# Optimization experiments

Measured on AMD Instinct MI355X. Metric: run time of the kernel, lower is better.

## Reference

```python
import jax, jax.numpy as jnp
import numpy as np

B, S, D = 2, 1024, 2048
L = 4
HQ, HKV, HD = 32, 8, 64
I = 5632
V = 32000
EPS = 1e-5
THETA = 10000.0
SCALE = HD ** -0.5
GROUP = HQ // HKV


def setup_inputs() -> dict:
    key = jax.random.key(0)
    ks = jax.random.split(key, 8)
    s = 0.02
    return {
        "input_ids": jax.random.randint(ks[0], (B, S), 0, V, dtype=jnp.int32),
        "positions": jnp.broadcast_to(jnp.arange(S, dtype=jnp.int32), (B, S)),
        "embed": jax.random.normal(ks[1], (V, D), jnp.float32) * s,
        "w_qkv": jax.random.normal(ks[2], (L, D, (HQ + 2 * HKV) * HD), jnp.float32) * s,
        "w_o": jax.random.normal(ks[3], (L, HQ * HD, D), jnp.float32) * s,
        "w_gate_up": jax.random.normal(ks[4], (L, D, 2 * I), jnp.float32) * s,
        "w_down": jax.random.normal(ks[5], (L, I, D), jnp.float32) * s,
        "ln1_w": jnp.ones((L, D), jnp.float32),
        "ln2_w": jnp.ones((L, D), jnp.float32),
        "norm_w": jnp.ones((D,), jnp.float32),
    }


def rmsnorm(x, w):
    var = jnp.mean(x * x, axis=-1, keepdims=True)
    return x * jax.lax.rsqrt(var + EPS) * w


def rope(positions, x):
    # x: [B, S, H, HD]; neox-style rotate-half RoPE
    inv_freq = 1.0 / (THETA ** (jnp.arange(0, HD, 2, dtype=jnp.float32) / HD))
    ang = positions.astype(jnp.float32)[..., None] * inv_freq  # [B, S, HD/2]
    cos = jnp.cos(ang)[:, :, None, :]
    sin = jnp.sin(ang)[:, :, None, :]
    x1, x2 = jnp.split(x, 2, axis=-1)
    return jnp.concatenate([x1 * cos - x2 * sin, x2 * cos + x1 * sin], axis=-1)


def llama_forward(input_ids, positions, embed, w_qkv, w_o, w_gate_up, w_down,
                  ln1_w, ln2_w, norm_w):
    h = embed[input_ids]                      # [B, S, D]
    res = jnp.zeros_like(h)
    causal = jnp.tril(jnp.ones((S, S), dtype=bool))
    neg = jnp.asarray(jnp.finfo(h.dtype).min, h.dtype)

    def layer(carry, params):
        h, res = carry
        wqkv, wo, wgu, wd, l1, l2 = params
        # fused RMSNorm + residual-add (vllm RMSNorm(x, residual) semantics)
        res = h + res
        h = rmsnorm(res, l1)
        # QKV projection + RoPE
        qkv = h @ wqkv
        q, k, v = jnp.split(qkv, [HQ * HD, (HQ + HKV) * HD], axis=-1)
        q = q.reshape(B, S, HQ, HD)
        k = k.reshape(B, S, HKV, HD)
        v = v.reshape(B, S, HKV, HD)
        q = rope(positions, q)
        k = rope(positions, k)
        # GQA: broadcast kv heads across query groups
        k = jnp.repeat(k, GROUP, axis=2)      # [B, S, HQ, HD]
        v = jnp.repeat(v, GROUP, axis=2)
        scores = jnp.einsum('bqhd,bkhd->bhqk', q, k) * SCALE
        scores = jnp.where(causal, scores, neg)
        attn = jax.nn.softmax(scores, axis=-1)
        o = jnp.einsum('bhqk,bkhd->bqhd', attn, v).reshape(B, S, HQ * HD)
        h = o @ wo
        # post-attention fused RMSNorm + residual
        res = h + res
        h = rmsnorm(res, l2)
        # SwiGLU MLP
        gu = h @ wgu
        g, u = jnp.split(gu, 2, axis=-1)
        h = (jax.nn.silu(g) * u) @ wd
        return (h, res), None

    (h, res), _ = jax.lax.scan(layer, (h, res),
                               (w_qkv, w_o, w_gate_up, w_down, ln1_w, ln2_w))
    return rmsnorm(h + res, norm_w)


def reference(input_ids, positions, embed, w_qkv, w_o, w_gate_up, w_down,
              ln1_w, ln2_w, norm_w):
    return llama_forward(input_ids, positions, embed, w_qkv, w_o, w_gate_up,
                         w_down, ln1_w, ln2_w, norm_w)
```

## Files before the change

kernel.cpp:

```cpp
#include <hip/hip_runtime.h>
#include <hip/hip_bf16.h>

#define B_ 2
#define S_ 1024
#define T_ (B_*S_)
#define D_ 2048
#define L_ 4
#define HQ_ 32
#define HKV_ 8
#define HD_ 64
#define I_ 5632
#define EPS_ 1e-5f
#define SCALE_ 0.125f

typedef __attribute__((ext_vector_type(4))) float  float4v;
typedef __attribute__((ext_vector_type(8))) short  short8v;

#define GLOAD16(g, l) \
  __builtin_amdgcn_global_load_lds((const __attribute__((address_space(1))) void*)(g), \
                                   (__attribute__((address_space(3))) void*)(l), 16, 0, 0)

__device__ __forceinline__ short f2bf(float f) {
  union { float f; unsigned u; } c; c.f = f;
  unsigned u = c.u + 0x7fffu + ((c.u >> 16) & 1u);
  return (short)(u >> 16);
}

__device__ __forceinline__ void xcd_swizzle(int gx, int gy, int& bx, int& by) {
  int nwg = gx * gy;
  int orig = by * gx + bx;
  int q = nwg >> 3, r = nwg & 7;
  int xcd = orig & 7, loc = orig >> 3;
  int swz = (xcd < r ? xcd * (q + 1) : r * (q + 1) + (xcd - r) * q) + loc;
  bx = swz / gy;
  by = swz - bx * gy;
}

__global__ __launch_bounds__(256)
void transpose_bf16(const float* __restrict__ in, short* __restrict__ out,
                    int K, int N) {
  __shared__ float t[64][65];
  const int bx = blockIdx.x * 64;
  const int by = blockIdx.y * 64;
  const int tid = threadIdx.x;
  const int lr = tid >> 4;
  const int lc = (tid & 15) * 4;
  #pragma unroll
  for (int j = 0; j < 64; j += 16) {
    float4v v = *(const float4v*)(in + (size_t)(by + lr + j) * N + bx + lc);
    t[lr + j][lc] = v[0]; t[lr + j][lc + 1] = v[1];
    t[lr + j][lc + 2] = v[2]; t[lr + j][lc + 3] = v[3];
  }
  __syncthreads();
  const int nr = tid >> 3;
  const int kc = (tid & 7) * 8;
  #pragma unroll
  for (int j = 0; j < 64; j += 32) {
    short8v y;
    #pragma unroll
    for (int e = 0; e < 8; e++) y[e] = f2bf(t[kc + e][nr + j]);
    *(short8v*)(out + (size_t)(bx + nr + j) * K + by + kc) = y;
  }
}

__global__ __launch_bounds__(256)
void embed_gather(const int* __restrict__ ids, const float* __restrict__ embed,
                  float* __restrict__ h) {
  size_t i = (size_t)blockIdx.x * 256 + threadIdx.x;
  int t  = (int)(i >> 9);
  int d4 = (int)(i & 511);
  ((float4v*)h)[i] = ((const float4v*)(embed + (size_t)ids[t] * D_))[d4];
}

__global__ __launch_bounds__(256)
void rmsnorm_add(const float* __restrict__ x, float* __restrict__ res,
                 const float* __restrict__ w, void* __restrict__ outp,
                 int first, int bf16out) {
  const int row = blockIdx.x;
  const int tid = threadIdx.x;
  const size_t base = (size_t)row * D_;
  float4v v0 = ((const float4v*)(x + base))[tid * 2];
  float4v v1 = ((const float4v*)(x + base))[tid * 2 + 1];
  if (!first) {
    v0 += ((const float4v*)(res + base))[tid * 2];
    v1 += ((const float4v*)(res + base))[tid * 2 + 1];
  }
  ((float4v*)(res + base))[tid * 2]     = v0;
  ((float4v*)(res + base))[tid * 2 + 1] = v1;
  float ss = v0[0]*v0[0] + v0[1]*v0[1] + v0[2]*v0[2] + v0[3]*v0[3]
           + v1[0]*v1[0] + v1[1]*v1[1] + v1[2]*v1[2] + v1[3]*v1[3];
  #pragma unroll
  for (int off = 32; off > 0; off >>= 1) ss += __shfl_xor(ss, off, 64);
  __shared__ float red[4];
  if ((tid & 63) == 0) red[tid >> 6] = ss;
  __syncthreads();
  float tot = red[0] + red[1] + red[2] + red[3];
  float rs = rsqrtf(tot * (1.0f / D_) + EPS_);
  float4v w0 = ((const float4v*)w)[tid * 2];
  float4v w1 = ((const float4v*)w)[tid * 2 + 1];
  float4v o0 = v0 * rs * w0;
  float4v o1 = v1 * rs * w1;
  if (bf16out) {
    short8v y;
    #pragma unroll
    for (int k = 0; k < 4; k++) { y[k] = f2bf(o0[k]); y[k + 4] = f2bf(o1[k]); }
    ((short8v*)((char*)outp + base * 2))[tid] = y;
  } else {
    float* op = (float*)outp + base;
    ((float4v*)op)[tid * 2]     = o0;
    ((float4v*)op)[tid * 2 + 1] = o1;
  }
}

#define BM 128
#define BN 128
#define BKS 32

__global__ __launch_bounds__(512, 2)
void gemm_big(const short* __restrict__ A, const short* __restrict__ Bt,
              float* __restrict__ C, int M, int N, int K) {
  __shared__ short sA[2][128 * 64];
  __shared__ short sB[2][256 * 64];
  int bx = blockIdx.x, by = blockIdx.y;
  xcd_swizzle(gridDim.x, gridDim.y, bx, by);
  const int tid  = threadIdx.x;
  const int lane = tid & 63;
  const int wv   = tid >> 6;
  const int wr   = wv >> 2;
  const int wc   = wv & 3;
  const int row0 = by * 128;
  const int col0 = bx * 256;
  const int fr = lane & 15;
  const int g  = lane >> 4;
  const int NT = K >> 6;

  float4v acc[4][4] = {};

  int rA[2], cA[2], rB[4], cB[4];
  #pragma unroll
  for (int k = 0; k < 2; k++) {
    int s = tid + k * 512;
    rA[k] = s >> 3;
    cA[k] = (((s & 7) ^ (rA[k] & 7)) << 3);
  }
  #pragma unroll
  for (int k = 0; k < 4; k++) {
    int s = tid + k * 512;
    rB[k] = s >> 3;
    cB[k] = (((s & 7) ^ (rB[k] & 7)) << 3);
  }

#define STAGEBIG(t, buf) do { \
    int k0_ = (t) << 6; \
    _Pragma("unroll") \
    for (int k_ = 0; k_ < 2; k_++) \
      GLOAD16(A  + (size_t)(row0 + rA[k_]) * K + k0_ + cA[k_], \
              &sA[buf][(tid + k_ * 512) * 8]); \
    _Pragma("unroll") \
    for (int k_ = 0; k_ < 4; k_++) \
      GLOAD16(Bt + (size_t)(col0 + rB[k_]) * K + k0_ + cB[k_], \
              &sB[buf][(tid + k_ * 512) * 8]); \
  } while (0)

  STAGEBIG(0, 0);

  for (int t = 0; t < NT; t++) {
    const int cur = t & 1;
    if (t + 1 < NT) {
      STAGEBIG(t + 1, cur ^ 1);
      asm volatile("s_waitcnt vmcnt(6)" ::: "memory");
    } else {
      asm volatile("s_waitcnt vmcnt(0)" ::: "memory");
    }
    __builtin_amdgcn_s_barrier();
    __builtin_amdgcn_sched_barrier(0);

    const short* pA = &sA[cur][(wr * 64) * 64];
    const short* pB = &sB[cur][(wc * 64) * 64];
    #pragma unroll
    for (int ks = 0; ks < 2; ks++) {
      const int fswk = ((((ks << 2) | g) ^ (fr & 7)) << 3);
      short8v bfr[4], afr[4];
      #pragma unroll
      for (int ni = 0; ni < 4; ni++)
        bfr[ni] = *(const short8v*)(pB + (ni * 16 + fr) * 64 + fswk);
      #pragma unroll
      for (int m4 = 0; m4 < 4; m4++)
        afr[m4] = *(const short8v*)(pA + (m4 * 16 + fr) * 64 + fswk);
      __builtin_amdgcn_s_setprio(1);
      #pragma unroll
      for (int m4 = 0; m4 < 4; m4++)
        #pragma unroll
        for (int ni = 0; ni < 4; ni++)
          acc[m4][ni] = __builtin_amdgcn_mfma_f32_16x16x32_bf16(
              afr[m4], bfr[ni], acc[m4][ni], 0, 0, 0);
      __builtin_amdgcn_s_setprio(0);
    }
    asm volatile("" ::: "memory");
    __builtin_amdgcn_s_barrier();
  }

  #pragma unroll
  for (int m4 = 0; m4 < 4; m4++)
    #pragma unroll
    for (int ni = 0; ni < 4; ni++) {
      size_t base = (size_t)(row0 + wr * 64 + m4 * 16 + g * 4) * N
                    + col0 + wc * 64 + ni * 16 + fr;
      #pragma unroll
      for (int r = 0; r < 4; r++)
        C[base + (size_t)r * N] = acc[m4][ni][r];
    }
#undef STAGEBIG
}

__global__ __launch_bounds__(256)
void gemm_n64(const short* __restrict__ A, const short* __restrict__ Bt,
              float* __restrict__ C, int M, int N, int K) {
  __shared__ short sA[BM * BKS];
  __shared__ short sB[64 * BKS];
  int bx = blockIdx.x, by = blockIdx.y;
  xcd_swizzle(gridDim.x, gridDim.y, bx, by);
  const int tid  = threadIdx.x;
  const int lane = tid & 63;
  const int wave = tid >> 6;
  const int wm = (wave >> 1) << 6;
  const int wn = (wave & 1) << 5;
  const int row0 = by * BM;
  const int col0 = bx * 64;
  const int fr = lane & 15;
  const int fk = (lane >> 4) << 3;
  float4v acc[4][2] = {};

  const int r_st  = tid >> 2;
  const int kc_st = (tid & 3) << 3;
  const short* pA = A  + (size_t)(row0 + r_st) * K + kc_st;
  const short* pB = Bt + (size_t)(col0 + r_st) * K + kc_st;
  const size_t stride64 = (size_t)64 * K;
  short* lA0 = &sA[tid * 8];
  short* lA1 = &sA[(256 + tid) * 8];
  short* lB0 = &sB[tid * 8];

  for (int k0 = 0; k0 < K; k0 += BKS) {
    GLOAD16(pA, lA0);
    GLOAD16(pA + stride64, lA1);
    GLOAD16(pB, lB0);
    pA += BKS; pB += BKS;
    __syncthreads();
    short8v af[4], bfr[2];
    #pragma unroll
    for (int f = 0; f < 4; f++)
      af[f] = *(const short8v*)(&sA[(wm + f * 16 + fr) * BKS + fk]);
    #pragma unroll
    for (int f = 0; f < 2; f++)
      bfr[f] = *(const short8v*)(&sB[(wn + f * 16 + fr) * BKS + fk]);
    #pragma unroll
    for (int i = 0; i < 4; i++)
      #pragma unroll
      for (int j = 0; j < 2; j++)
        acc[i][j] = __builtin_amdgcn_mfma_f32_16x16x32_bf16(af[i], bfr[j], acc[i][j], 0, 0, 0);
    __syncthreads();
  }
  const int cr = (lane >> 4) << 2;
  const int cc = lane & 15;
  #pragma unroll
  for (int i = 0; i < 4; i++)
    #pragma unroll
    for (int j = 0; j < 2; j++) {
      size_t base = (size_t)(row0 + wm + i * 16 + cr) * N + col0 + wn + j * 16 + cc;
      #pragma unroll
      for (int r = 0; r < 4; r++)
        C[base + (size_t)r * N] = acc[i][j][r];
    }
}

__global__ __launch_bounds__(256)
void gemm_qkv_rope(const short* __restrict__ A, const short* __restrict__ Bt,
                   const float* __restrict__ tab, short* __restrict__ qbf,
                   short* __restrict__ kbf, short* __restrict__ vbf, int K) {
  __shared__ short sA[BM * BKS];
  __shared__ short sB[BN * BKS];
  int bx = blockIdx.x, by = blockIdx.y;
  xcd_swizzle(gridDim.x, gridDim.y, bx, by);
  const int tid  = threadIdx.x;
  const int lane = tid & 63;
  const int wave = tid >> 6;
  const int wm = (wave >> 1) << 6;
  const int wn = (wave & 1) << 6;
  const int row0 = by * BM;
  const int col0 = bx * BN;
  const int fr = lane & 15;
  const int fk = (lane >> 4) << 3;
  float4v acc[4][4] = {};

  const int r_st  = tid >> 2;
  const int kc_st = (tid & 3) << 3;
  const short* pA = A  + (size_t)(row0 + r_st) * K + kc_st;
  const short* pB = Bt + (size_t)(col0 + r_st) * K + kc_st;
  const size_t stride64 = (size_t)64 * K;
  short* lA0 = &sA[tid * 8];
  short* lA1 = &sA[(256 + tid) * 8];
  short* lB0 = &sB[tid * 8];
  short* lB1 = &sB[(256 + tid) * 8];

  for (int k0 = 0; k0 < K; k0 += BKS) {
    GLOAD16(pA, lA0);
    GLOAD16(pA + stride64, lA1);
    GLOAD16(pB, lB0);
    GLOAD16(pB + stride64, lB1);
    pA += BKS; pB += BKS;
    __syncthreads();
    short8v af[4], bfr[4];
    #pragma unroll
    for (int f = 0; f < 4; f++) {
      af[f]  = *(const short8v*)(&sA[(wm + f * 16 + fr) * BKS + fk]);
      bfr[f] = *(const short8v*)(&sB[(wn + f * 16 + fr) * BKS + fk]);
    }
    #pragma unroll
    for (int i = 0; i < 4; i++)
      #pragma unroll
      for (int j = 0; j < 4; j++)
        acc[i][j] = __builtin_amdgcn_mfma_f32_16x16x32_bf16(af[i], bfr[j], acc[i][j], 0, 0, 0);
    __syncthreads();
  }
  const int cr = (lane >> 4) << 2;
  const int cc = lane & 15;
  const int head = (col0 + wn) >> 6;

  if (head < HQ_ + HKV_) {
    const float sc = (head < HQ_) ? SCALE_ : 1.0f;
    #pragma unroll
    for (int i = 0; i < 4; i++)
      #pragma unroll
      for (int jj = 0; jj < 2; jj++)
        #pragma unroll
        for (int r = 0; r < 4; r++) {
          int m = row0 + wm + i * 16 + cr + r;
          int b = m >> 10, s = m & (S_ - 1);
          int d1 = jj * 16 + cc;
          float x1 = acc[i][jj][r], x2 = acc[i][jj + 2][r];
          const float* tb = tab + (size_t)m * 64 + d1 * 2;
          float c = tb[0], sn = tb[1];
          short y1 = f2bf((x1 * c - x2 * sn) * sc);
          short y2 = f2bf((x2 * c + x1 * sn) * sc);
          size_t base;
          if (head < HQ_)
            base = ((size_t)((b * HQ_ + head) * S_ + s)) * HD_;
          else
            base = ((size_t)((b * HKV_ + head - HQ_) * S_ + s)) * HD_;
          short* dst = (head < HQ_) ? qbf : kbf;
          dst[base + d1]      = y1;
          dst[base + d1 + 32] = y2;
        }
  } else {
    const int vh = head - HQ_ - HKV_;
    #pragma unroll
    for (int i = 0; i < 4; i++)
      #pragma unroll
      for (int j = 0; j < 4; j++)
        #pragma unroll
        for (int r = 0; r < 4; r++) {
          int m = row0 + wm + i * 16 + cr + r;
          int b = m >> 10, s = m & (S_ - 1);
          vbf[((size_t)((b * HKV_ + vh) * S_ + s)) * HD_ + j * 16 + cc] =
              f2bf(acc[i][j][r]);
        }
  }
}

__global__ __launch_bounds__(256)
void swiglu_kernel(const float* __restrict__ gu, short* __restrict__ mlp) {
  size_t i = (size_t)blockIdx.x * 256 + threadIdx.x;
  size_t t = i / 704;
  int c = (int)(i - t * 704);
  const float* gp = gu + t * 11264 + c * 8;
  const float* up = gp + 5632;
  float4v g0 = *(const float4v*)gp, g1 = *(const float4v*)(gp + 4);
  float4v u0 = *(const float4v*)up, u1 = *(const float4v*)(up + 4);
  short8v r;
  #pragma unroll
  for (int k = 0; k < 4; k++) {
    r[k]     = f2bf(g0[k] / (1.0f + __expf(-g0[k])) * u0[k]);
    r[k + 4] = f2bf(g1[k] / (1.0f + __expf(-g1[k])) * u1[k]);
  }
  ((short8v*)mlp)[i] = r;
}

__global__ __launch_bounds__(256)
void rope_table(const int* __restrict__ pos, float* __restrict__ tab) {
  int i = blockIdx.x * 256 + threadIdx.x;
  int t = i >> 5, ii = i & 31;
  float p = (float)pos[t];
  float freq = __expf(-(float)ii * (9.210340371976184f / 32.0f));
  float ang = p * freq;
  tab[2 * i]     = cosf(ang);
  tab[2 * i + 1] = sinf(ang);
}

#define KPAD 68

__global__ __launch_bounds__(256)
void transpose_v(const short* __restrict__ vbf, short* __restrict__ vtbf) {
  __shared__ short sv[64 * KPAD];
  const int jt = blockIdx.x, kh = blockIdx.y, b = blockIdx.z;
  const int tid = threadIdx.x;
  const short* src = vbf + ((size_t)((b * HKV_ + kh) * S_ + jt * 64)) * HD_;
  #pragma unroll
  for (int it = 0; it < 2; it++) {
    int c = it * 256 + tid;
    int rr = c >> 3, ch = (c & 7) * 8;
    *(short8v*)(&sv[rr * KPAD + ch]) = *(const short8v*)(src + (size_t)rr * HD_ + ch);
  }
  __syncthreads();
  const int dc = tid >> 2;
  const int jc = (tid & 3) * 16;
  short8v o1, o2;
  #pragma unroll
  for (int k = 0; k < 8; k++) o1[k] = sv[(jc + k) * KPAD + dc];
  #pragma unroll
  for (int k = 0; k < 8; k++) o2[k] = sv[(jc + 8 + k) * KPAD + dc];
  short* od = vtbf + ((size_t)((b * HKV_ + kh) * HD_ + dc)) * S_ + jt * 64 + jc;
  *(short8v*)od       = o1;
  *(short8v*)(od + 8) = o2;
}

__global__ __launch_bounds__(256)
void attn_mfma(const short* __restrict__ qbf, const short* __restrict__ kbf,
               const short* __restrict__ vtbf, short* __restrict__ obf) {
  __shared__ short sK[64 * KPAD];
  __shared__ short sVt[64 * KPAD];
  __shared__ short sP[4][16 * KPAD];
  const int qb = blockIdx.x;
  const int h  = blockIdx.y;
  const int b  = blockIdx.z;
  const int kh = h >> 2;
  const int tid  = threadIdx.x;
  const int lane = tid & 63;
  const int wv   = tid >> 6;
  const int q0 = qb * 64;
  const int cc = lane & 15;
  const int g  = lane >> 4;

  short8v qf0, qf1;
  {
    const short* qrow = qbf + ((size_t)((b * HQ_ + h) * S_ + q0 + wv * 16 + cc)) * HD_;
    qf0 = *(const short8v*)(qrow + g * 8);
    qf1 = *(const short8v*)(qrow + g * 8 + 32);
  }
  float4v accO[4] = {};
  float m_r[4], l_r[4];
  #pragma unroll
  for (int r = 0; r < 4; r++) { m_r[r] = -1e30f; l_r[r] = 0.f; }

  const short* kb = kbf  + ((size_t)(b * HKV_ + kh)) * S_ * HD_;
  const short* vb = vtbf + ((size_t)(b * HKV_ + kh)) * HD_ * S_;

  for (int jt = 0; jt <= qb; jt++) {
    const int j0 = jt * 64;
    #pragma unroll
    for (int it = 0; it < 2; it++) {
      int idx = it * 256 + tid;
      int rr = idx >> 3, ch = (idx & 7) * 8;
      *(short8v*)(&sK[rr * KPAD + ch])  = *(const short8v*)(kb + (size_t)(j0 + rr) * HD_ + ch);
      *(short8v*)(&sVt[rr * KPAD + ch]) = *(const short8v*)(vb + (size_t)rr * S_ + j0 + ch);
    }
    __syncthreads();

    float4v sc[4] = {};
    #pragma unroll
    for (int ct = 0; ct < 4; ct++) {
      short8v k0 = *(const short8v*)(&sK[(ct * 16 + cc) * KPAD + g * 8]);
      short8v k1 = *(const short8v*)(&sK[(ct * 16 + cc) * KPAD + g * 8 + 32]);
      sc[ct] = __builtin_amdgcn_mfma_f32_16x16x32_bf16(qf0, k0, sc[ct], 0, 0, 0);
      sc[ct] = __builtin_amdgcn_mfma_f32_16x16x32_bf16(qf1, k1, sc[ct], 0, 0, 0);
    }
    if (jt == qb) {
      #pragma unroll
      for (int ct = 0; ct < 4; ct++)
        #pragma unroll
        for (int r = 0; r < 4; r++)
          if (j0 + ct * 16 + cc > q0 + wv * 16 + g * 4 + r) sc[ct][r] = -1e30f;
    }
    float corr[4];
    #pragma unroll
    for (int r = 0; r < 4; r++) {
      float pm = fmaxf(fmaxf(sc[0][r], sc[1][r]), fmaxf(sc[2][r], sc[3][r]));
      pm = fmaxf(pm, __shfl_xor(pm, 1, 64));
      pm = fmaxf(pm, __shfl_xor(pm, 2, 64));
      pm = fmaxf(pm, __shfl_xor(pm, 4, 64));
      pm = fmaxf(pm, __shfl_xor(pm, 8, 64));
      float mn = fmaxf(m_r[r], pm);
      corr[r] = __expf(m_r[r] - mn);
      m_r[r] = mn;
      float rs = 0.f;
      #pragma unroll
      for (int ct = 0; ct < 4; ct++) {
        float p = __expf(sc[ct][r] - mn);
        sc[ct][r] = p;
        rs += p;
      }
      rs += __shfl_xor(rs, 1, 64);
      rs += __shfl_xor(rs, 2, 64);
      rs += __shfl_xor(rs, 4, 64);
      rs += __shfl_xor(rs, 8, 64);
      l_r[r] = l_r[r] * corr[r] + rs;
    }
    #pragma unroll
    for (int ct = 0; ct < 4; ct++)
      #pragma unroll
      for (int r = 0; r < 4; r++)
        sP[wv][(g * 4 + r) * KPAD + ct * 16 + cc] = f2bf(sc[ct][r]);
    #pragma unroll
    for (int dt = 0; dt < 4; dt++)
      #pragma unroll
      for (int r = 0; r < 4; r++)
        accO[dt][r] *= corr[r];
    short8v pf0 = *(const short8v*)(&sP[wv][cc * KPAD + g * 8]);
    short8v pf1 = *(const short8v*)(&sP[wv][cc * KPAD + g * 8 + 32]);
    #pragma unroll
    for (int dt = 0; dt < 4; dt++) {
      short8v v0 = *(const short8v*)(&sVt[(dt * 16 + cc) * KPAD + g * 8]);
      short8v v1 = *(const short8v*)(&sVt[(dt * 16 + cc) * KPAD + g * 8 + 32]);
      accO[dt] = __builtin_amdgcn_mfma_f32_16x16x32_bf16(pf0, v0, accO[dt], 0, 0, 0);
      accO[dt] = __builtin_amdgcn_mfma_f32_16x16x32_bf16(pf1, v1, accO[dt], 0, 0, 0);
    }
    __syncthreads();
  }
  #pragma unroll
  for (int dt = 0; dt < 4; dt++)
    #pragma unroll
    for (int r = 0; r < 4; r++) {
      int q = q0 + wv * 16 + g * 4 + r;
      obf[((size_t)(b * S_ + q)) * 2048 + h * 64 + dt * 16 + cc] = f2bf(accO[dt][r] / l_r[r]);
    }
}

extern "C" void kernel_launch(void* const* d_in, const int* in_sizes, int n_in,
                              void* d_out, int out_size, void* d_ws, size_t ws_size,
                              hipStream_t stream) {
  const int*   ids   = (const int*)d_in[0];
  const int*   pos   = (const int*)d_in[1];
  const float* embed = (const float*)d_in[2];
  const float* w_qkv = (const float*)d_in[3];
  const float* w_o   = (const float*)d_in[4];
  const float* w_gu  = (const float*)d_in[5];
  const float* w_dn  = (const float*)d_in[6];
  const float* ln1   = (const float*)d_in[7];
  const float* ln2   = (const float*)d_in[8];
  const float* normw = (const float*)d_in[9];
  float* out = (float*)d_out;

  char* p = (char*)d_ws;
  short* wT    = (short*)p; p += (size_t)11264 * 2048 * 2;
  float* h     = (float*)p; p += (size_t)T_ * D_ * 4;
  float* res   = (float*)p; p += (size_t)T_ * D_ * 4;
  short* hnbf  = (short*)p; p += (size_t)T_ * D_ * 2;
  short* obf   = (short*)p; p += (size_t)T_ * D_ * 2;
  short* mlpbf = (short*)p; p += (size_t)T_ * I_ * 2;
  float* tab   = (float*)p; p += (size_t)T_ * 64 * 4;
  short* qbf   = (short*)p; p += (size_t)B_ * HQ_ * S_ * HD_ * 2;
  short* kbf   = (short*)p; p += (size_t)B_ * HKV_ * S_ * HD_ * 2;
  short* vbf   = (short*)p; p += (size_t)B_ * HKV_ * S_ * HD_ * 2;
  short* vtbf  = (short*)p; p += (size_t)B_ * HKV_ * HD_ * S_ * 2;
  float* gu    = (float*)p; p += (size_t)T_ * 2 * I_ * 4;

  embed_gather<<<T_ * D_ / 4 / 256, 256, 0, stream>>>(ids, embed, h);
  rope_table<<<T_ * 32 / 256, 256, 0, stream>>>(pos, tab);

  for (int l = 0; l < L_; l++) {
    rmsnorm_add<<<T_, 256, 0, stream>>>(h, res, ln1 + l * D_, hnbf, l == 0 ? 1 : 0, 1);

    transpose_bf16<<<dim3(3072 / 64, 2048 / 64), 256, 0, stream>>>(
        w_qkv + (size_t)l * 2048 * 3072, wT, 2048, 3072);
    gemm_qkv_rope<<<dim3(3072 / BN, T_ / BM), 256, 0, stream>>>(
        hnbf, wT, tab, qbf, kbf, vbf, 2048);

    transpose_v<<<dim3(16, 8, 2), 256, 0, stream>>>(vbf, vtbf);
    attn_mfma<<<dim3(16, 32, 2), 256, 0, stream>>>(qbf, kbf, vtbf, obf);

    transpose_bf16<<<dim3(2048 / 64, 2048 / 64), 256, 0, stream>>>(
        w_o + (size_t)l * 2048 * 2048, wT, 2048, 2048);
    gemm_n64<<<dim3(2048 / 64, T_ / BM), 256, 0, stream>>>(
        obf, wT, h, T_, 2048, 2048);

    rmsnorm_add<<<T_, 256, 0, stream>>>(h, res, ln2 + l * D_, hnbf, 0, 1);

    transpose_bf16<<<dim3(11264 / 64, 2048 / 64), 256, 0, stream>>>(
        w_gu + (size_t)l * 2048 * 11264, wT, 2048, 11264);
    gemm_big<<<dim3(11264 / 256, T_ / 128), 512, 0, stream>>>(
        hnbf, wT, gu, T_, 11264, 2048);

    swiglu_kernel<<<T_ * I_ / 8 / 256, 256, 0, stream>>>(gu, mlpbf);

    transpose_bf16<<<dim3(2048 / 64, 5632 / 64), 256, 0, stream>>>(
        w_dn + (size_t)l * 5632 * 2048, wT, 5632, 2048);
    gemm_n64<<<dim3(2048 / 64, T_ / BM), 256, 0, stream>>>(
        mlpbf, wT, h, T_, 2048, 5632);
  }
  rmsnorm_add<<<T_, 256, 0, stream>>>(h, res, normw, out, 0, 0);
}
```

Measured before the change: 2.017 ms.

## Fuse SwiGLU into gate/up GEMM epilogue and use pipelined 128x128 GEMM for N=2048

The gate/up GEMM now loads matching gate and up weight tiles, keeps two accumulators, and applies silu(g)*u in the epilogue, writing bf16 MLP activations directly. This removes the large fp32 gu intermediate buffer and the separate swiglu kernel pass. The o-proj and down-proj GEMMs switch from the simple 64-wide single-buffered kernel to a double-buffered 512-thread 128x128 variant with swizzled LDS and async global-to-LDS loads. The trade-off is more LDS and registers per block in the fused kernel, and fewer blocks (256) for the N=2048 GEMMs, which may leave some CUs idle.

Result: faster. 1.828 ms (-9.4%).

```diff
diff --git a/kernel.cpp b/kernel.cpp
--- a/kernel.cpp
+++ b/kernel.cpp
@@ -116,11 +116,11 @@
 #define BN 128
 #define BKS 32
 
-__global__ __launch_bounds__(512, 2)
-void gemm_big(const short* __restrict__ A, const short* __restrict__ Bt,
-              float* __restrict__ C, int M, int N, int K) {
+__global__ __launch_bounds__(512, 4)
+void gemm_big128(const short* __restrict__ A, const short* __restrict__ Bt,
+                 float* __restrict__ C, int M, int N, int K) {
   __shared__ short sA[2][128 * 64];
-  __shared__ short sB[2][256 * 64];
+  __shared__ short sB[2][128 * 64];
   int bx = blockIdx.x, by = blockIdx.y;
   xcd_swizzle(gridDim.x, gridDim.y, bx, by);
   const int tid  = threadIdx.x;
@@ -129,46 +129,40 @@
   const int wr   = wv >> 2;
   const int wc   = wv & 3;
   const int row0 = by * 128;
-  const int col0 = bx * 256;
+  const int col0 = bx * 128;
   const int fr = lane & 15;
   const int g  = lane >> 4;
   const int NT = K >> 6;
 
-  float4v acc[4][4] = {};
-
-  int rA[2], cA[2], rB[4], cB[4];
+  float4v acc[4][2] = {};
+
+  int rS[2], cS[2];
   #pragma unroll
   for (int k = 0; k < 2; k++) {
     int s = tid + k * 512;
-    rA[k] = s >> 3;
-    cA[k] = (((s & 7) ^ (rA[k] & 7)) << 3);
-  }
-  #pragma unroll
-  for (int k = 0; k < 4; k++) {
-    int s = tid + k * 512;
-    rB[k] = s >> 3;
-    cB[k] = (((s & 7) ^ (rB[k] & 7)) << 3);
-  }
-
-#define STAGEBIG(t, buf) do { \
+    rS[k] = s >> 3;
+    cS[k] = (((s & 7) ^ (rS[k] & 7)) << 3);
+  }
+
+#define STAGE128(t, buf) do { \
     int k0_ = (t) << 6; \
     _Pragma("unroll") \
     for (int k_ = 0; k_ < 2; k_++) \
-      GLOAD16(A  + (size_t)(row0 + rA[k_]) * K + k0_ + cA[k_], \
+      GLOAD16(A  + (size_t)(row0 + rS[k_]) * K + k0_ + cS[k_], \
               &sA[buf][(tid + k_ * 512) * 8]); \
     _Pragma("unroll") \
-    for (int k_ = 0; k_ < 4; k_++) \
-      GLOAD16(Bt + (size_t)(col0 + rB[k_]) * K + k0_ + cB[k_], \
+    for (int k_ = 0; k_ < 2; k_++) \
+      GLOAD16(Bt + (size_t)(col0 + rS[k_]) * K + k0_ + cS[k_], \
               &sB[buf][(tid + k_ * 512) * 8]); \
   } while (0)
 
-  STAGEBIG(0, 0);
+  STAGE128(0, 0);
 
   for (int t = 0; t < NT; t++) {
     const int cur = t & 1;
     if (t + 1 < NT) {
-      STAGEBIG(t + 1, cur ^ 1);
-      asm volatile("s_waitcnt vmcnt(6)" ::: "memory");
+      STAGE128(t + 1, cur ^ 1);
+      asm volatile("s_waitcnt vmcnt(4)" ::: "memory");
     } else {
       asm volatile("s_waitcnt vmcnt(0)" ::: "memory");
     }
@@ -176,13 +170,13 @@
     __builtin_amdgcn_sched_barrier(0);
 
     const short* pA = &sA[cur][(wr * 64) * 64];
-    const short* pB = &sB[cur][(wc * 64) * 64];
+    const short* pB = &sB[cur][(wc * 32) * 64];
     #pragma unroll
     for (int ks = 0; ks < 2; ks++) {
       const int fswk = ((((ks << 2) | g) ^ (fr & 7)) << 3);
-      short8v bfr[4], afr[4];
-      #pragma unroll
-      for (int ni = 0; ni < 4; ni++)
+      short8v bfr[2], afr[4];
+      #pragma unroll
+      for (int ni = 0; ni < 2; ni++)
         bfr[ni] = *(const short8v*)(pB + (ni * 16 + fr) * 64 + fswk);
       #pragma unroll
       for (int m4 = 0; m4 < 4; m4++)
@@ -191,7 +185,7 @@
       #pragma unroll
       for (int m4 = 0; m4 < 4; m4++)
         #pragma unroll
-        for (int ni = 0; ni < 4; ni++)
+        for (int ni = 0; ni < 2; ni++)
           acc[m4][ni] = __builtin_amdgcn_mfma_f32_16x16x32_bf16(
               afr[m4], bfr[ni], acc[m4][ni], 0, 0, 0);
       __builtin_amdgcn_s_setprio(0);
@@ -203,74 +197,119 @@
   #pragma unroll
   for (int m4 = 0; m4 < 4; m4++)
     #pragma unroll
-    for (int ni = 0; ni < 4; ni++) {
+    for (int ni = 0; ni < 2; ni++) {
       size_t base = (size_t)(row0 + wr * 64 + m4 * 16 + g * 4) * N
-                    + col0 + wc * 64 + ni * 16 + fr;
+                    + col0 + wc * 32 + ni * 16 + fr;
       #pragma unroll
       for (int r = 0; r < 4; r++)
         C[base + (size_t)r * N] = acc[m4][ni][r];
     }
-#undef STAGEBIG
-}
-
-__global__ __launch_bounds__(256)
-void gemm_n64(const short* __restrict__ A, const short* __restrict__ Bt,
-              float* __restrict__ C, int M, int N, int K) {
-  __shared__ short sA[BM * BKS];
-  __shared__ short sB[64 * BKS];
+#undef STAGE128
+}
+
+__global__ __launch_bounds__(512, 2)
+void gemm_glu_big(const short* __restrict__ A, const short* __restrict__ Bt,
+                  short* __restrict__ mlp, int K) {
+  __shared__ short sA[2][128 * 64];
+  __shared__ short sG[2][128 * 64];
+  __shared__ short sU[2][128 * 64];
   int bx = blockIdx.x, by = blockIdx.y;
   xcd_swizzle(gridDim.x, gridDim.y, bx, by);
   const int tid  = threadIdx.x;
   const int lane = tid & 63;
-  const int wave = tid >> 6;
-  const int wm = (wave >> 1) << 6;
-  const int wn = (wave & 1) << 5;
-  const int row0 = by * BM;
-  const int col0 = bx * 64;
+  const int wv   = tid >> 6;
+  const int wr   = wv >> 2;
+  const int wc   = wv & 3;
+  const int row0 = by * 128;
+  const int col0 = bx * 128;
   const int fr = lane & 15;
-  const int fk = (lane >> 4) << 3;
-  float4v acc[4][2] = {};
-
-  const int r_st  = tid >> 2;
-  const int kc_st = (tid & 3) << 3;
-  const short* pA = A  + (size_t)(row0 + r_st) * K + kc_st;
-  const short* pB = Bt + (size_t)(col0 + r_st) * K + kc_st;
-  const size_t stride64 = (size_t)64 * K;
-  short* lA0 = &sA[tid * 8];
-  short* lA1 = &sA[(256 + tid) * 8];
-  short* lB0 = &sB[tid * 8];
-
-  for (int k0 = 0; k0 < K; k0 += BKS) {
-    GLOAD16(pA, lA0);
-    GLOAD16(pA + stride64, lA1);
-    GLOAD16(pB, lB0);
-    pA += BKS; pB += BKS;
-    __syncthreads();
-    short8v af[4], bfr[2];
-    #pragma unroll
-    for (int f = 0; f < 4; f++)
-      af[f] = *(const short8v*)(&sA[(wm + f * 16 + fr) * BKS + fk]);
-    #pragma unroll
-    for (int f = 0; f < 2; f++)
-      bfr[f] = *(const short8v*)(&sB[(wn + f * 16 + fr) * BKS + fk]);
-    #pragma unroll
-    for (int i = 0; i < 4; i++)
-      #pragma unroll
-      for (int j = 0; j < 2; j++)
-        acc[i][j] = __builtin_amdgcn_mfma_f32_16x16x32_bf16(af[i], bfr[j], acc[i][j], 0, 0, 0);
-    __syncthreads();
-  }
-  const int cr = (lane >> 4) << 2;
-  const int cc = lane & 15;
-  #pragma unroll
-  for (int i = 0; i < 4; i++)
-    #pragma unroll
-    for (int j = 0; j < 2; j++) {
-      size_t base = (size_t)(row0 + wm + i * 16 + cr) * N + col0 + wn + j * 16 + cc;
-      #pragma unroll
-      for (int r = 0; r < 4; r++)
-        C[base + (size_t)r * N] = acc[i][j][r];
-    }
+  const int g  = lane >> 4;
+  const int NT = K >> 6;
+
+  float4v accg[4][2] = {};
+  float4v accu[4][2] = {};
+
+  int rS[2], cS[2];
+  #pragma unroll
+  for (int k = 0; k < 2; k++) {
+    int s = tid + k * 512;
+    rS[k] = s >> 3;
+    cS[k] = (((s & 7) ^ (rS[k] & 7)) << 3);
+  }
+
+#define STAGEGLU(t, buf) do { \
+    int k0_ = (t) << 6; \
+    _Pragma("unroll") \
+    for (int k_ = 0; k_ < 2; k_++) \
+      GLOAD16(A  + (size_t)(row0 + rS[k_]) * K + k0_ + cS[k_], \
+              &sA[buf][(tid + k_ * 512) * 8]); \
+    _Pragma("unroll") \
+    for (int k_ = 0; k_ < 2; k_++) \
+      GLOAD16(Bt + (size_t)(col0 + rS[k_]) * K + k0_ + cS[k_], \
+              &sG[buf][(tid + k_ * 512) * 8]); \
+    _Pragma("unroll") \
+    for (int k_ = 0; k_ < 2; k_++) \
+      GLOAD16(Bt + (size_t)(col0 + I_ + rS[k_]) * K + k0_ + cS[k_], \
+              &sU[buf][(tid + k_ * 512) * 8]); \
+  } while (0)
+
+  STAGEGLU(0, 0);
+
+  for (int t = 0; t < NT; t++) {
+    const int cur = t & 1;
+    if (t + 1 < NT) {
+      STAGEGLU(t + 1, cur ^ 1);
+      asm volatile("s_waitcnt vmcnt(6)" ::: "memory");
+    } else {
+      asm volatile("s_waitcnt vmcnt(0)" ::: "memory");
+    }
+    __builtin_amdgcn_s_barrier();
+    __builtin_amdgcn_sched_barrier(0);
+
+    const short* pA = &sA[cur][(wr * 64) * 64];
+    const short* pG = &sG[cur][(wc * 32) * 64];
+    const short* pU = &sU[cur][(wc * 32) * 64];
+    #pragma unroll
+    for (int ks = 0; ks < 2; ks++) {
+      const int fswk = ((((ks << 2) | g) ^ (fr & 7)) << 3);
+      short8v bg[2], bu[2], afr[4];
+      #pragma unroll
+      for (int ni = 0; ni < 2; ni++) {
+        bg[ni] = *(const short8v*)(pG + (ni * 16 + fr) * 64 + fswk);
+        bu[ni] = *(const short8v*)(pU + (ni * 16 + fr) * 64 + fswk);
+      }
+      #pragma unroll
+      for (int m4 = 0; m4 < 4; m4++)
+        afr[m4] = *(const short8v*)(pA + (m4 * 16 + fr) * 64 + fswk);
+      __builtin_amdgcn_s_setprio(1);
+      #pragma unroll
+      for (int m4 = 0; m4 < 4; m4++)
+        #pragma unroll
+        for (int ni = 0; ni < 2; ni++) {
+          accg[m4][ni] = __builtin_amdgcn_mfma_f32_16x16x32_bf16(
+              afr[m4], bg[ni], accg[m4][ni], 0, 0, 0);
+          accu[m4][ni] = __builtin_amdgcn_mfma_f32_16x16x32_bf16(
+              afr[m4], bu[ni], accu[m4][ni], 0, 0, 0);
+        }
+      __builtin_amdgcn_s_setprio(0);
+    }
+    asm volatile("" ::: "memory");
+    __builtin_amdgcn_s_barrier();
+  }
+
+  #pragma unroll
+  for (int m4 = 0; m4 < 4; m4++)
+    #pragma unroll
+    for (int ni = 0; ni < 2; ni++) {
+      size_t base = (size_t)(row0 + wr * 64 + m4 * 16 + g * 4) * I_
+                    + col0 + wc * 32 + ni * 16 + fr;
+      #pragma unroll
+      for (int r = 0; r < 4; r++) {
+        float gv = accg[m4][ni][r], uv = accu[m4][ni][r];
+        mlp[base + (size_t)r * I_] = f2bf(gv / (1.0f + __expf(-gv)) * uv);
+      }
+    }
+#undef STAGEGLU
 }
 
 __global__ __launch_bounds__(256)
@@ -368,24 +407,6 @@
 }
 
 __global__ __launch_bounds__(256)
-void swiglu_kernel(const float* __restrict__ gu, short* __restrict__ mlp) {
-  size_t i = (size_t)blockIdx.x * 256 + threadIdx.x;
-  size_t t = i / 704;
-  int c = (int)(i - t * 704);
-  const float* gp = gu + t * 11264 + c * 8;
-  const float* up = gp + 5632;
-  float4v g0 = *(const float4v*)gp, g1 = *(const float4v*)(gp + 4);
-  float4v u0 = *(const float4v*)up, u1 = *(const float4v*)(up + 4);
-  short8v r;
-  #pragma unroll
-  for (int k = 0; k < 4; k++) {
-    r[k]     = f2bf(g0[k] / (1.0f + __expf(-g0[k])) * u0[k]);
-    r[k + 4] = f2bf(g1[k] / (1.0f + __expf(-g1[k])) * u1[k]);
-  }
-  ((short8v*)mlp)[i] = r;
-}
-
-__global__ __launch_bounds__(256)
 void rope_table(const int* __restrict__ pos, float* __restrict__ tab) {
   int i = blockIdx.x * 256 + threadIdx.x;
   int t = i >> 5, ii = i & 31;
@@ -561,7 +582,6 @@
   short* kbf   = (short*)p; p += (size_t)B_ * HKV_ * S_ * HD_ * 2;
   short* vbf   = (short*)p; p += (size_t)B_ * HKV_ * S_ * HD_ * 2;
   short* vtbf  = (short*)p; p += (size_t)B_ * HKV_ * HD_ * S_ * 2;
-  float* gu    = (float*)p; p += (size_t)T_ * 2 * I_ * 4;
 
   embed_gather<<<T_ * D_ / 4 / 256, 256, 0, stream>>>(ids, embed, h);
   rope_table<<<T_ * 32 / 256, 256, 0, stream>>>(pos, tab);
@@ -579,21 +599,19 @@
 
     transpose_bf16<<<dim3(2048 / 64, 2048 / 64), 256, 0, stream>>>(
         w_o + (size_t)l * 2048 * 2048, wT, 2048, 2048);
-    gemm_n64<<<dim3(2048 / 64, T_ / BM), 256, 0, stream>>>(
+    gemm_big128<<<dim3(2048 / 128, T_ / 128), 512, 0, stream>>>(
         obf, wT, h, T_, 2048, 2048);
 
     rmsnorm_add<<<T_, 256, 0, stream>>>(h, res, ln2 + l * D_, hnbf, 0, 1);
 
     transpose_bf16<<<dim3(11264 / 64, 2048 / 64), 256, 0, stream>>>(
         w_gu + (size_t)l * 2048 * 11264, wT, 2048, 11264);
-    gemm_big<<<dim3(11264 / 256, T_ / 128), 512, 0, stream>>>(
-        hnbf, wT, gu, T_, 11264, 2048);
-
-    swiglu_kernel<<<T_ * I_ / 8 / 256, 256, 0, stream>>>(gu, mlpbf);
+    gemm_glu_big<<<dim3(I_ / 128, T_ / 128), 512, 0, stream>>>(
+        hnbf, wT, mlpbf, 2048);
 
     transpose_bf16<<<dim3(2048 / 64, 5632 / 64), 256, 0, stream>>>(
         w_dn + (size_t)l * 5632 * 2048, wT, 5632, 2048);
-    gemm_n64<<<dim3(2048 / 64, T_ / BM), 256, 0, stream>>>(
+    gemm_big128<<<dim3(2048 / 128, T_ / 128), 512, 0, stream>>>(
         mlpbf, wT, h, T_, 2048, 5632);
   }
   rmsnorm_add<<<T_, 256, 0, stream>>>(h, res, normw, out, 0, 0);
```
